# Performance work log

Hardware: AMD Instinct MI355X
Metric: run time of the kernel (lower is better)

The kernel has to match this reference:

```python
import jax, jax.numpy as jnp
import numpy as np

SOBEL_X = jnp.array([[-1., 0., 1.], [-2., 0., 2.], [-1., 0., 1.]], dtype=jnp.float32)
LAP = jnp.array([[1., 2., 1.], [2., -12., 2.], [1., 2., 1.]], dtype=jnp.float32)
UPDATE_RATE = 0.5


def _perchannel_conv(x, filters):
    # x: [B,C,H,W]; filters: [F,3,3]; circular pad, depthwise conv with F outputs per channel
    B, C, H, W = x.shape
    Fk = filters.shape[0]
    xp = jnp.pad(x, ((0, 0), (0, 0), (1, 1), (1, 1)), mode='wrap')
    # kernel[c*Fk + f] = filters[f] -> output channel order [c0f0,c0f1,c0f2,c1f0,...] matching torch reshape
    k = jnp.broadcast_to(filters[None], (C, Fk, 3, 3)).reshape(C * Fk, 1, 3, 3)
    return jax.lax.conv_general_dilated(xp, k, (1, 1), 'VALID',
                                        feature_group_count=C,
                                        dimension_numbers=('NCHW', 'OIHW', 'NCHW'))


def _unfold27(x):
    # circular pad over (C,H,W) then gather the 27-neighborhood: [B,C,H,W] -> [B,C,27,H,W]
    B, C, H, W = x.shape
    p = jnp.pad(x, ((0, 0), (1, 1), (1, 1), (1, 1)), mode='wrap')
    shifts = [p[:, dc:dc + C, dh:dh + H, dw:dw + W]
              for dc in range(3) for dh in range(3) for dw in range(3)]
    return jnp.stack(shifts, axis=2)


def setup_inputs() -> dict:
    key = jax.random.key(0)
    kx, km, k1, kb, k2 = jax.random.split(key, 5)
    B, C, H, W, HID = 4, 16, 512, 512, 128
    x = jax.random.normal(kx, (B, C, H, W), dtype=jnp.float32)
    rand_mask = jax.random.uniform(km, (B, 1, H, W), dtype=jnp.float32)
    w1_w = jax.random.normal(k1, (HID, 4 * C), dtype=jnp.float32) * 0.05
    w1_b = jax.random.normal(kb, (HID,), dtype=jnp.float32) * 0.05
    w2_w = jax.random.normal(k2, (C, HID), dtype=jnp.float32) * 0.05
    return {"x": x, "rand_mask": rand_mask, "w1_w": w1_w, "w1_b": w1_b, "w2_w": w2_w}


def reference(x, rand_mask, w1_w, w1_b, w2_w):
    filters = jnp.stack([SOBEL_X, SOBEL_X.T, LAP])  # [3,3,3]
    obs = _perchannel_conv(x, filters)              # [B,3C,H,W]
    percep = jnp.concatenate([x, obs], axis=1)      # [B,4C,H,W]
    h = jax.nn.relu(jnp.einsum('bchw,kc->bkhw', percep, w1_w) + w1_b[None, :, None, None])
    y = jnp.einsum('bkhw,ck->bchw', h, w2_w)        # [B,C,H,W]

    update_mask = jnp.floor(rand_mask + UPDATE_RATE)
    x_mass, x_normal = x[:, :3], x[:, 3:]
    y_mass, y_normal = y[:, :3], y[:, 3:]

    Aff = jnp.exp(y_mass * 0.1)                     # [B,3,H,W], strictly positive
    E = _unfold27(Aff).sum(axis=2)                  # total affinity of each cell's 27-neighborhood
    E_n = _unfold27(E)                              # neighbor normalizers
    S_n = _unfold27(x_mass)                         # neighbor masses
    new_mass = (Aff[:, :, None] / E_n * S_n).sum(axis=2)  # mass-conserving redistribution

    new_normal = x_normal + y_normal * update_mask
    return jnp.concatenate([new_mass, new_normal], axis=1)
```

## Files before the change

kernel.cpp:

```cpp
#include <hip/hip_runtime.h>

#define HW (512*512)
#define WMASK 511

typedef short bf16x8 __attribute__((ext_vector_type(8)));
typedef float f32x4 __attribute__((ext_vector_type(4)));
typedef unsigned int u32x4 __attribute__((ext_vector_type(4)));

__device__ __forceinline__ unsigned short f2bf(float f) {
    union { float f; unsigned int u; } v; v.f = f;
    unsigned int r = (v.u + 0x7FFFu + ((v.u >> 16) & 1u)) >> 16;
    return (unsigned short)r;
}
__device__ __forceinline__ int corig(int c) {
    int s8 = c >> 3, b = (c >> 2) & 1, f = c & 3;
    int ch = 2*s8 + b;
    return (f == 0) ? ch : (16 + ch*3 + (f - 1));
}

__global__ __launch_bounds__(256) void nca_prep(
    const float* __restrict__ w1w, const float* __restrict__ w1b,
    const float* __restrict__ w2w, unsigned int* __restrict__ wbuf)
{
    int tid = threadIdx.x;
    for (int u = tid; u < 4096; u += 256) {
        int m2 = u >> 8, ln = (u >> 2) & 63, d = u & 3;
        int m = m2 >> 1, ks = m2 & 1;
        int qq = ln >> 4, row = ln & 15;
        int c0 = ks*32 + qq*8 + 2*d;
        int hr = m*16 + row;
        unsigned int lo = f2bf(w1w[hr*64 + corig(c0)]);
        unsigned int hi = f2bf(w1w[hr*64 + corig(c0+1)]);
        wbuf[u] = lo | (hi << 16);
    }
    for (int u = tid; u < 1024; u += 256) {
        int s = u >> 8, ln = (u >> 2) & 63, d = u & 3;
        int qq = ln >> 4, ych = ln & 15;
        int k0 = s*32 + qq*8 + 2*d;
        unsigned int lo = f2bf(w2w[ych*128 + k0]);
        unsigned int hi = f2bf(w2w[ych*128 + k0 + 1]);
        wbuf[4096 + u] = lo | (hi << 16);
    }
    if (tid < 128) {
        union { float f; unsigned int u; } v; v.f = w1b[tid];
        wbuf[5120 + tid] = v.u;
    }
}

__global__ __launch_bounds__(256) void nca_mlp_mfma(
    const float* __restrict__ x,
    const float* __restrict__ rmask,
    const unsigned int* __restrict__ wbuf,
    float* __restrict__ out,
    float* __restrict__ SA)
{
    __shared__ __align__(16) unsigned int wsh[5248];
    int tid  = threadIdx.x;
    int lane = tid & 63;
    int wv   = tid >> 6;
    int q    = lane >> 4;
    int r    = lane & 15;

    {
        const u32x4* src = (const u32x4*)wbuf;
        u32x4* dst = (u32x4*)wsh;
#pragma unroll
        for (int u = 0; u < 6; ++u) {
            int idx = tid + u*256;
            if (idx < 1312) dst[idx] = src[idx];
        }
    }

    int bIdx = blockIdx.x >> 10;
    int rem  = blockIdx.x & 1023;
    int hrow = ((rem >> 3) << 2) + wv;
    int w0   = (rem & 7) << 6;
    int c4   = w0 + (r << 2);
    int cl   = (c4 - 1) & WMASK;
    int cr   = (c4 + 4) & WMASK;
    int rm = ((hrow-1)&WMASK)<<9, rc = hrow<<9, rp = ((hrow+1)&WMASK)<<9;
    const float* xb = x + bIdx*16*HW;

    union PFU { unsigned short s[8]; bf16x8 v; } pf[4][2];
#pragma unroll
    for (int ks = 0; ks < 2; ++ks) {
#pragma unroll
        for (int b2 = 0; b2 < 2; ++b2) {
            const float* pl = xb + (8*ks + 2*q + b2)*HW;
            f32x4 m0 = *(const f32x4*)(pl + rm + c4);
            f32x4 m1 = *(const f32x4*)(pl + rc + c4);
            f32x4 m2 = *(const f32x4*)(pl + rp + c4);
            float col[6][3];
            col[0][0] = pl[rm+cl]; col[0][1] = pl[rc+cl]; col[0][2] = pl[rp+cl];
#pragma unroll
            for (int j = 0; j < 4; ++j) {
                col[j+1][0] = m0[j]; col[j+1][1] = m1[j]; col[j+1][2] = m2[j];
            }
            col[5][0] = pl[rm+cr]; col[5][1] = pl[rc+cr]; col[5][2] = pl[rp+cr];
#pragma unroll
            for (int p = 0; p < 4; ++p) {
                float a00 = col[p][0],   a01 = col[p+1][0], a02 = col[p+2][0];
                float a10 = col[p][1],   a11 = col[p+1][1], a12 = col[p+2][1];
                float a20 = col[p][2],   a21 = col[p+1][2], a22 = col[p+2][2];
                float sx = (a02 - a00) + 2.f*(a12 - a10) + (a22 - a20);
                float sy = (a20 - a00) + 2.f*(a21 - a01) + (a22 - a02);
                float lp = a00 + 2.f*a01 + a02
                         + 2.f*a10 - 12.f*a11 + 2.f*a12
                         + a20 + 2.f*a21 + a22;
                pf[p][ks].s[b2*4+0] = (unsigned short)f2bf(a11);
                pf[p][ks].s[b2*4+1] = (unsigned short)f2bf(sx);
                pf[p][ks].s[b2*4+2] = (unsigned short)f2bf(sy);
                pf[p][ks].s[b2*4+3] = (unsigned short)f2bf(lp);
            }
        }
    }

    __syncthreads();

    const unsigned short* w1s = (const unsigned short*)wsh;
    const unsigned short* w2s = (const unsigned short*)(wsh + 4096);
    const float* w1bs = (const float*)(wsh + 5120);

    f32x4 yacc[4];
#pragma unroll
    for (int P = 0; P < 4; ++P) { yacc[P][0]=0.f; yacc[P][1]=0.f; yacc[P][2]=0.f; yacc[P][3]=0.f; }

#pragma unroll
    for (int s = 0; s < 4; ++s) {
        f32x4 Hc[2][4];
#pragma unroll
        for (int t = 0; t < 2; ++t)
#pragma unroll
            for (int P = 0; P < 4; ++P) { Hc[t][P][0]=0.f; Hc[t][P][1]=0.f; Hc[t][P][2]=0.f; Hc[t][P][3]=0.f; }

#pragma unroll
        for (int t = 0; t < 2; ++t) {
#pragma unroll
            for (int ks = 0; ks < 2; ++ks) {
                bf16x8 af = *(const bf16x8*)&w1s[(((2*s+t)*2 + ks)*64 + lane)*8];
#pragma unroll
                for (int P = 0; P < 4; ++P)
                    Hc[t][P] = __builtin_amdgcn_mfma_f32_16x16x32_bf16(af, pf[P][ks].v, Hc[t][P], 0, 0, 0);
            }
        }

        bf16x8 wf = *(const bf16x8*)&w2s[(s*64 + lane)*8];
        float bi0[2][4];
#pragma unroll
        for (int t = 0; t < 2; ++t) {
            const float* bp = &w1bs[(2*s+t)*16 + (q<<2)];
#pragma unroll
            for (int i = 0; i < 4; ++i) bi0[t][i] = bp[i];
        }

        int ga = ((q & 1) << 5) | r;
        int gb = ga + 16;
        bool hiT = (q >= 2);

#pragma unroll
        for (int P = 0; P < 4; ++P) {
            unsigned int pk00, pk01, pk10, pk11;
            {
                f32x4 hv = Hc[0][P];
                float h0 = fmaxf(hv[0] + bi0[0][0], 0.f);
                float h1 = fmaxf(hv[1] + bi0[0][1], 0.f);
                float h2 = fmaxf(hv[2] + bi0[0][2], 0.f);
                float h3 = fmaxf(hv[3] + bi0[0][3], 0.f);
                pk00 = (unsigned int)f2bf(h0) | ((unsigned int)f2bf(h1) << 16);
                pk01 = (unsigned int)f2bf(h2) | ((unsigned int)f2bf(h3) << 16);
            }
            {
                f32x4 hv = Hc[1][P];
                float h0 = fmaxf(hv[0] + bi0[1][0], 0.f);
                float h1 = fmaxf(hv[1] + bi0[1][1], 0.f);
                float h2 = fmaxf(hv[2] + bi0[1][2], 0.f);
                float h3 = fmaxf(hv[3] + bi0[1][3], 0.f);
                pk10 = (unsigned int)f2bf(h0) | ((unsigned int)f2bf(h1) << 16);
                pk11 = (unsigned int)f2bf(h2) | ((unsigned int)f2bf(h3) << 16);
            }
            unsigned int s00 = (unsigned int)__shfl((int)pk00, ga);
            unsigned int s10 = (unsigned int)__shfl((int)pk10, ga);
            unsigned int s01 = (unsigned int)__shfl((int)pk01, ga);
            unsigned int s11 = (unsigned int)__shfl((int)pk11, ga);
            unsigned int s02 = (unsigned int)__shfl((int)pk00, gb);
            unsigned int s12 = (unsigned int)__shfl((int)pk10, gb);
            unsigned int s03 = (unsigned int)__shfl((int)pk01, gb);
            unsigned int s13 = (unsigned int)__shfl((int)pk11, gb);
            union { unsigned int u[4]; bf16x8 v; } bb;
            bb.u[0] = hiT ? s10 : s00;
            bb.u[1] = hiT ? s11 : s01;
            bb.u[2] = hiT ? s12 : s02;
            bb.u[3] = hiT ? s13 : s03;
            yacc[P] = __builtin_amdgcn_mfma_f32_16x16x32_bf16(wf, bb.v, yacc[P], 0, 0, 0);
        }
    }

    int pbase = rc + c4;
    f32x4 mk = *(const f32x4*)(rmask + bIdx*HW + pbase);
#pragma unroll
    for (int i = 0; i < 4; ++i) mk[i] = floorf(mk[i] + 0.5f);
    float* ob = out + bIdx*16*HW;

    if (q == 0) {
        f32x4 sacc;
#pragma unroll
        for (int i = 0; i < 3; ++i) {
            f32x4 A;
#pragma unroll
            for (int P = 0; P < 4; ++P) A[P] = expf(0.1f * yacc[P][i]);
            *(f32x4*)(ob + i*HW + pbase) = A;
            if (i == 0) sacc = A; else sacc += A;
        }
        *(f32x4*)(SA + bIdx*HW + pbase) = sacc;
        f32x4 yv;
#pragma unroll
        for (int P = 0; P < 4; ++P) yv[P] = yacc[P][3];
        f32x4 xv = *(const f32x4*)(xb + 3*HW + pbase);
        *(f32x4*)(ob + 3*HW + pbase) = xv + yv*mk;
    } else {
#pragma unroll
        for (int i = 0; i < 4; ++i) {
            int ch = 4*q + i;
            f32x4 yv;
#pragma unroll
            for (int P = 0; P < 4; ++P) yv[P] = yacc[P][i];
            f32x4 xv = *(const f32x4*)(xb + ch*HW + pbase);
            *(f32x4*)(ob + ch*HW + pbase) = xv + yv*mk;
        }
    }
}

__global__ __launch_bounds__(256) void nca_bc(
    const float* __restrict__ x,
    const float* __restrict__ SA,
    float* __restrict__ out)
{
    __shared__ float sa[12][69];
    __shared__ float tt[10][67];
    int tid = threadIdx.x;
    int bb = blockIdx.x >> 9;
    int t2 = blockIdx.x & 511;
    int h0 = (t2 >> 3) << 3;
    int w0 = (t2 & 7) << 6;
    const float* sab = SA + bb*HW;

    for (int e = tid; e < 816; e += 256) {
        int rr = e / 68, cc = e - rr*68;
        int gh = (h0 + rr - 2) & WMASK, gw = (w0 + cc - 2) & WMASK;
        sa[rr][cc] = sab[(gh<<9) | gw];
    }
    __syncthreads();

    const float* xb = x + bb*16*HW;
    for (int e = tid; e < 660; e += 256) {
        int rr = e / 66, cc = e - rr*66;
        float E = sa[rr  ][cc] + sa[rr  ][cc+1] + sa[rr  ][cc+2]
                + sa[rr+1][cc] + sa[rr+1][cc+1] + sa[rr+1][cc+2]
                + sa[rr+2][cc] + sa[rr+2][cc+1] + sa[rr+2][cc+2];
        int gh = (h0 + rr - 1) & WMASK, gw = (w0 + cc - 1) & WMASK;
        int g = (gh<<9) | gw;
        float Sm = xb[g] + xb[HW + g] + xb[2*HW + g];
        tt[rr][cc] = Sm / E;
    }
    __syncthreads();

    for (int e = tid; e < 512; e += 256) {
        int rr = e >> 6, cc = e & 63;
        float R = tt[rr  ][cc] + tt[rr  ][cc+1] + tt[rr  ][cc+2]
                + tt[rr+1][cc] + tt[rr+1][cc+1] + tt[rr+1][cc+2]
                + tt[rr+2][cc] + tt[rr+2][cc+1] + tt[rr+2][cc+2];
        int p = ((h0 + rr) << 9) | (w0 + cc);
        float* ob = out + bb*16*HW + p;
        ob[0]    *= R;
        ob[HW]   *= R;
        ob[2*HW] *= R;
    }
}

extern "C" void kernel_launch(void* const* d_in, const int* in_sizes, int n_in,
                              void* d_out, int out_size, void* d_ws, size_t ws_size,
                              hipStream_t stream) {
    const float* x     = (const float*)d_in[0];
    const float* rmask = (const float*)d_in[1];
    const float* w1w   = (const float*)d_in[2];
    const float* w1b   = (const float*)d_in[3];
    const float* w2w   = (const float*)d_in[4];
    float* out = (float*)d_out;

    float* SA = (float*)d_ws;
    unsigned int* wbuf = (unsigned int*)((char*)d_ws + 4*HW*sizeof(float));

    hipLaunchKernelGGL(nca_prep,     dim3(1),    dim3(256), 0, stream, w1w, w1b, w2w, wbuf);
    hipLaunchKernelGGL(nca_mlp_mfma, dim3(4096), dim3(256), 0, stream, x, rmask, wbuf, out, SA);
    hipLaunchKernelGGL(nca_bc,       dim3(2048), dim3(256), 0, stream, x, SA, out);
}
```

Baseline: 187.1 us.

## Use hardware bf16 pack, LDS hidden transpose, and precomputed mass sum buffer

Replaces software bf16 rounding with the packed v_cvt_pk_bf16_f32 instruction in both the feature and hidden-activation paths. Replaces eight cross-lane shuffles per tile with a swizzled LDS write/read to re-layout hidden activations for the second MFMA. Also has the MLP kernel write a per-pixel sum of the three mass channels to a new workspace buffer, so the redistribution kernel reads one plane instead of three strided x planes. This costs extra LDS, an additional global write, and relies on unsynchronized per-wave LDS reuse within a wave.

```diff
diff --git a/kernel.cpp b/kernel.cpp
--- a/kernel.cpp
+++ b/kernel.cpp
@@ -11,6 +11,11 @@
     union { float f; unsigned int u; } v; v.f = f;
     unsigned int r = (v.u + 0x7FFFu + ((v.u >> 16) & 1u)) >> 16;
     return (unsigned short)r;
+}
+__device__ __forceinline__ unsigned int CVT(float lo, float hi) {
+    unsigned int r;
+    asm("v_cvt_pk_bf16_f32 %0, %1, %2" : "=v"(r) : "v"(lo), "v"(hi));
+    return r;
 }
 __device__ __forceinline__ int corig(int c) {
     int s8 = c >> 3, b = (c >> 2) & 1, f = c & 3;
@@ -52,9 +57,11 @@
     const float* __restrict__ rmask,
     const unsigned int* __restrict__ wbuf,
     float* __restrict__ out,
-    float* __restrict__ SA)
+    float* __restrict__ SA,
+    float* __restrict__ SM)
 {
     __shared__ __align__(16) unsigned int wsh[5248];
+    __shared__ __align__(16) unsigned int hx[4][4][256];
     int tid  = threadIdx.x;
     int lane = tid & 63;
     int wv   = tid >> 6;
@@ -81,7 +88,8 @@
     int rm = ((hrow-1)&WMASK)<<9, rc = hrow<<9, rp = ((hrow+1)&WMASK)<<9;
     const float* xb = x + bIdx*16*HW;
 
-    union PFU { unsigned short s[8]; bf16x8 v; } pf[4][2];
+    union PFU { unsigned int u[4]; bf16x8 v; } pf[4][2];
+    f32x4 c_sav0, c_sav1;
 #pragma unroll
     for (int ks = 0; ks < 2; ++ks) {
 #pragma unroll
@@ -90,6 +98,7 @@
             f32x4 m0 = *(const f32x4*)(pl + rm + c4);
             f32x4 m1 = *(const f32x4*)(pl + rc + c4);
             f32x4 m2 = *(const f32x4*)(pl + rp + c4);
+            if (ks == 0) { if (b2 == 0) c_sav0 = m1; else c_sav1 = m1; }
             float col[6][3];
             col[0][0] = pl[rm+cl]; col[0][1] = pl[rc+cl]; col[0][2] = pl[rp+cl];
 #pragma unroll
@@ -107,10 +116,8 @@
                 float lp = a00 + 2.f*a01 + a02
                          + 2.f*a10 - 12.f*a11 + 2.f*a12
                          + a20 + 2.f*a21 + a22;
-                pf[p][ks].s[b2*4+0] = (unsigned short)f2bf(a11);
-                pf[p][ks].s[b2*4+1] = (unsigned short)f2bf(sx);
-                pf[p][ks].s[b2*4+2] = (unsigned short)f2bf(sy);
-                pf[p][ks].s[b2*4+3] = (unsigned short)f2bf(lp);
+                pf[p][ks].u[2*b2]   = CVT(a11, sx);
+                pf[p][ks].u[2*b2+1] = CVT(sy, lp);
             }
         }
     }
@@ -121,6 +128,13 @@
     const unsigned short* w2s = (const unsigned short*)(wsh + 4096);
     const float* w1bs = (const float*)(wsh + 5120);
 
+    unsigned int* hbase = &hx[wv][0][0];
+    int k8a = (q >> 1);
+    int k8b = 2 + (q >> 1);
+    int wi0 = k8a*64 + ((r ^ k8a) << 2) + ((q & 1) << 1);
+    int wi1 = k8b*64 + ((r ^ k8b) << 2) + ((q & 1) << 1);
+    int ri  = q*64 + ((r ^ q) << 2);
+
     f32x4 yacc[4];
 #pragma unroll
     for (int P = 0; P < 4; ++P) { yacc[P][0]=0.f; yacc[P][1]=0.f; yacc[P][2]=0.f; yacc[P][3]=0.f; }
@@ -152,10 +166,6 @@
 #pragma unroll
             for (int i = 0; i < 4; ++i) bi0[t][i] = bp[i];
         }
-
-        int ga = ((q & 1) << 5) | r;
-        int gb = ga + 16;
-        bool hiT = (q >= 2);
 
 #pragma unroll
         for (int P = 0; P < 4; ++P) {
@@ -166,8 +176,7 @@
                 float h1 = fmaxf(hv[1] + bi0[0][1], 0.f);
                 float h2 = fmaxf(hv[2] + bi0[0][2], 0.f);
                 float h3 = fmaxf(hv[3] + bi0[0][3], 0.f);
-                pk00 = (unsigned int)f2bf(h0) | ((unsigned int)f2bf(h1) << 16);
-                pk01 = (unsigned int)f2bf(h2) | ((unsigned int)f2bf(h3) << 16);
+                pk00 = CVT(h0, h1); pk01 = CVT(h2, h3);
             }
             {
                 f32x4 hv = Hc[1][P];
@@ -175,23 +184,18 @@
                 float h1 = fmaxf(hv[1] + bi0[1][1], 0.f);
                 float h2 = fmaxf(hv[2] + bi0[1][2], 0.f);
                 float h3 = fmaxf(hv[3] + bi0[1][3], 0.f);
-                pk10 = (unsigned int)f2bf(h0) | ((unsigned int)f2bf(h1) << 16);
-                pk11 = (unsigned int)f2bf(h2) | ((unsigned int)f2bf(h3) << 16);
-            }
-            unsigned int s00 = (unsigned int)__shfl((int)pk00, ga);
-            unsigned int s10 = (unsigned int)__shfl((int)pk10, ga);
-            unsigned int s01 = (unsigned int)__shfl((int)pk01, ga);
-            unsigned int s11 = (unsigned int)__shfl((int)pk11, ga);
-            unsigned int s02 = (unsigned int)__shfl((int)pk00, gb);
-            unsigned int s12 = (unsigned int)__shfl((int)pk10, gb);
-            unsigned int s03 = (unsigned int)__shfl((int)pk01, gb);
-            unsigned int s13 = (unsigned int)__shfl((int)pk11, gb);
-            union { unsigned int u[4]; bf16x8 v; } bb;
-            bb.u[0] = hiT ? s10 : s00;
-            bb.u[1] = hiT ? s11 : s01;
-            bb.u[2] = hiT ? s12 : s02;
-            bb.u[3] = hiT ? s13 : s03;
-            yacc[P] = __builtin_amdgcn_mfma_f32_16x16x32_bf16(wf, bb.v, yacc[P], 0, 0, 0);
+                pk10 = CVT(h0, h1); pk11 = CVT(h2, h3);
+            }
+            unsigned int* hb = hbase + P*256;
+            *reinterpret_cast<unsigned long long*>(&hb[wi0]) =
+                (unsigned long long)pk00 | ((unsigned long long)pk01 << 32);
+            *reinterpret_cast<unsigned long long*>(&hb[wi1]) =
+                (unsigned long long)pk10 | ((unsigned long long)pk11 << 32);
+        }
+#pragma unroll
+        for (int P = 0; P < 4; ++P) {
+            bf16x8 bv = *reinterpret_cast<const bf16x8*>(&hbase[P*256 + ri]);
+            yacc[P] = __builtin_amdgcn_mfma_f32_16x16x32_bf16(wf, bv, yacc[P], 0, 0, 0);
         }
     }
 
@@ -212,6 +216,8 @@
             if (i == 0) sacc = A; else sacc += A;
         }
         *(f32x4*)(SA + bIdx*HW + pbase) = sacc;
+        f32x4 x2v = *(const f32x4*)(xb + 2*HW + pbase);
+        *(f32x4*)(SM + bIdx*HW + pbase) = c_sav0 + c_sav1 + x2v;
         f32x4 yv;
 #pragma unroll
         for (int P = 0; P < 4; ++P) yv[P] = yacc[P][3];
@@ -231,8 +237,8 @@
 }
 
 __global__ __launch_bounds__(256) void nca_bc(
-    const float* __restrict__ x,
     const float* __restrict__ SA,
+    const float* __restrict__ SM,
     float* __restrict__ out)
 {
     __shared__ float sa[12][69];
@@ -243,6 +249,7 @@
     int h0 = (t2 >> 3) << 3;
     int w0 = (t2 & 7) << 6;
     const float* sab = SA + bb*HW;
+    const float* smb = SM + bb*HW;
 
     for (int e = tid; e < 816; e += 256) {
         int rr = e / 68, cc = e - rr*68;
@@ -251,7 +258,6 @@
     }
     __syncthreads();
 
-    const float* xb = x + bb*16*HW;
     for (int e = tid; e < 660; e += 256) {
         int rr = e / 66, cc = e - rr*66;
         float E = sa[rr  ][cc] + sa[rr  ][cc+1] + sa[rr  ][cc+2]
@@ -259,8 +265,7 @@
                 + sa[rr+2][cc] + sa[rr+2][cc+1] + sa[rr+2][cc+2];
         int gh = (h0 + rr - 1) & WMASK, gw = (w0 + cc - 1) & WMASK;
         int g = (gh<<9) | gw;
-        float Sm = xb[g] + xb[HW + g] + xb[2*HW + g];
-        tt[rr][cc] = Sm / E;
+        tt[rr][cc] = smb[g] / E;
     }
     __syncthreads();
 
@@ -288,9 +293,10 @@
     float* out = (float*)d_out;
 
     float* SA = (float*)d_ws;
-    unsigned int* wbuf = (unsigned int*)((char*)d_ws + 4*HW*sizeof(float));
+    float* SM = SA + 4*HW;
+    unsigned int* wbuf = (unsigned int*)((char*)d_ws + 8*HW*sizeof(float));
 
     hipLaunchKernelGGL(nca_prep,     dim3(1),    dim3(256), 0, stream, w1w, w1b, w2w, wbuf);
-    hipLaunchKernelGGL(nca_mlp_mfma, dim3(4096), dim3(256), 0, stream, x, rmask, wbuf, out, SA);
-    hipLaunchKernelGGL(nca_bc,       dim3(2048), dim3(256), 0, stream, x, SA, out);
-}
+    hipLaunchKernelGGL(nca_mlp_mfma, dim3(4096), dim3(256), 0, stream, x, rmask, wbuf, out, SA, SM);
+    hipLaunchKernelGGL(nca_bc,       dim3(2048), dim3(256), 0, stream, SA, SM, out);
+}
```

Result: no change. 184.1 us (-1.6%).
